# Performance work log

Measured on AMD Instinct MI355X. Metric: run time of the kernel, lower is better.

## Reference

```python
import jax, jax.numpy as jnp
import numpy as np

CONF = 0.25
IOU = 0.7
MAX_DET = 300
IMG_H = 1280
IMG_W = 1280
KPT_SHAPE = (17, 3)
MAX_NMS = 3000
BS = 16
N_ANCH = 33600  # (1280/8)^2 + (1280/16)^2 + (1280/32)^2


def setup_inputs() -> dict:
    key = jax.random.key(0)
    k1, k2, k3, k4 = jax.random.split(key, 4)
    # realistic YOLO head outputs: centers in image, positive w/h, conf in (0,1)
    cxy = jax.random.uniform(k1, (BS, 2, N_ANCH)) * jnp.array([IMG_W, IMG_H], jnp.float32).reshape(1, 2, 1)
    wh = jax.random.uniform(k2, (BS, 2, N_ANCH)) * 200.0 + 4.0
    conf = jax.random.uniform(k3, (BS, 1, N_ANCH))
    kpts = jax.random.uniform(k4, (BS, 51, N_ANCH)) * float(IMG_W)
    preds = jnp.concatenate([cxy, wh, conf, kpts], axis=1).astype(jnp.float32)
    return {"preds": preds}


def _pairwise_iou(boxes):
    # boxes: [M, 4] xyxy
    area = (boxes[:, 2] - boxes[:, 0]) * (boxes[:, 3] - boxes[:, 1])
    lt = jnp.maximum(boxes[:, None, :2], boxes[None, :, :2])
    rb = jnp.minimum(boxes[:, None, 2:], boxes[None, :, 2:])
    wh = jnp.clip(rb - lt, 0.0)
    inter = wh[..., 0] * wh[..., 1]
    return inter / (area[:, None] + area[None, :] - inter + 1e-9)


def _nms_keep(boxes, valid):
    # greedy NMS over score-descending boxes; returns bool keep mask [M]
    M = boxes.shape[0]
    idx = jnp.arange(M)
    supp = (_pairwise_iou(boxes) > IOU) & (idx[None, :] > idx[:, None])

    def body(i, keep):
        # row i suppresses later boxes only if it is itself kept
        return keep & ~(supp[i] & keep[i])

    return jax.lax.fori_loop(0, M, body, valid)


def _per_image(boxes_xywh, scores, kpts):
    # boxes_xywh: [N,4], scores: [N], kpts: [N,51]
    valid = scores > CONF
    masked = jnp.where(valid, scores, -1.0)
    order = jnp.argsort(-masked)[:MAX_NMS]  # top max_nms by score, desc
    b = boxes_xywh[order]
    sc = scores[order]
    kp = kpts[order]
    v = valid[order]
    # xywh -> xyxy with clip to image bounds
    cx, cy, w, h = b[:, 0], b[:, 1], b[:, 2], b[:, 3]
    x1 = jnp.clip(cx - w / 2, 0.0, IMG_W)
    y1 = jnp.clip(cy - h / 2, 0.0, IMG_H)
    x2 = jnp.clip(cx + w / 2, 0.0, IMG_W)
    y2 = jnp.clip(cy + h / 2, 0.0, IMG_H)
    bxy = jnp.stack([x1, y1, x2, y2], axis=-1)
    # faithful to original _clip_coords quirk: only channels 0 and 1 of the 51 clipped
    kp = kp.at[:, 0].set(jnp.clip(kp[:, 0], 0.0, IMG_W))
    kp = kp.at[:, 1].set(jnp.clip(kp[:, 1], 0.0, IMG_H))
    keep = _nms_keep(bxy, v)
    rank = jnp.cumsum(keep) - 1
    sel = keep & (rank < MAX_DET)
    tgt = jnp.where(sel, rank, MAX_DET)  # dropped rows scatter to slot MAX_DET (sliced off)
    ob = jnp.zeros((MAX_DET + 1, 4), bxy.dtype).at[tgt].set(jnp.where(sel[:, None], bxy, 0.0))[:MAX_DET]
    osc = jnp.zeros((MAX_DET + 1, 1), sc.dtype).at[tgt].set(jnp.where(sel[:, None], sc[:, None], 0.0))[:MAX_DET]
    okp = jnp.zeros((MAX_DET + 1, 51), kp.dtype).at[tgt].set(jnp.where(sel[:, None], kp, 0.0))[:MAX_DET]
    return ob, osc, okp


def reference(preds):
    bs = preds.shape[0]
    x = jnp.transpose(preds, (0, 2, 1))  # [bs, N, 56]
    ob, osc, okp = jax.vmap(_per_image)(x[..., :4], x[..., 4], x[..., 5:])
    return ob, osc, okp.reshape(bs, MAX_DET, *KPT_SHAPE)
```

## Files before the change

### kernel.cpp

```cpp
#include <hip/hip_runtime.h>
#include <stdint.h>

#define N_ANCH 33600
#define BS 16
#define NCH 56
#define MAX_NMS 3000
#define MAX_DET 300
#define CONF_T 0.25f
#define IOU_T 0.7f
#define IMG 1280.0f
#define NW 47
#define NBINS 4096
#define HIST_BINS 4097
#define CAP 4096
#define WCAP 4096
#define WC_STRIDE 16
#define NIT 9

#define OFF_CAND 0
#define OFF_WL   (OFF_CAND + BS*CAP*8)
#define OFF_META (OFF_WL + BS*WCAP*4)
#define OFF_BOX  ((OFF_META + BS*MAX_NMS*8 + 15) & ~15)
#define OFF_WC   (OFF_BOX + BS*MAX_NMS*16)
#define OFF_GBM  (OFF_WC + BS*WC_STRIDE*4)
#define OFF_FOI  (OFF_GBM + BS*8)

__device__ __forceinline__ int score_bucket(float c, uint32_t* bits_out) {
    if (!(c > CONF_T)) { *bits_out = 0u; return 0; }
    uint32_t bits = __float_as_uint(c);
    *bits_out = bits;
    int bucket = (int)(bits >> 12) - 0x3E800 + 1;
    bucket = bucket < 1 ? 1 : (bucket > NBINS ? NBINS : bucket);
    return bucket;
}

__device__ __forceinline__ float iou_pair(float4 bi, float ai, float4 bj) {
    float aj  = (bj.z - bj.x) * (bj.w - bj.y);
    float ltx = fmaxf(bi.x, bj.x), lty = fmaxf(bi.y, bj.y);
    float rbx = fminf(bi.z, bj.z), rby = fminf(bi.w, bj.w);
    float wx  = fmaxf(rbx - ltx, 0.f), wy = fmaxf(rby - lty, 0.f);
    float inter = wx * wy;
    return inter / (ai + aj - inter + 1e-9f);
}

__device__ __forceinline__ unsigned long long readlane64(unsigned long long v, int lane) {
    uint32_t lo = (uint32_t)v, hi = (uint32_t)(v >> 32);
    uint32_t rlo = __builtin_amdgcn_readlane(lo, lane);
    uint32_t rhi = __builtin_amdgcn_readlane(hi, lane);
    return ((unsigned long long)rhi << 32) | (unsigned long long)rlo;
}

__global__ void __launch_bounds__(1024)
k_phase1(const float* __restrict__ preds,
         unsigned long long* __restrict__ cand,
         unsigned int* __restrict__ wlist, int* __restrict__ wcount,
         int2* __restrict__ gbm) {
    __shared__ int hl[HIST_BINS];
    __shared__ int st[HIST_BINS];
    __shared__ int part[256];
    __shared__ int suf[256];
    __shared__ int ldsB, ldsM, ldsWc;
    const int b = blockIdx.x, t = threadIdx.x;
    if (t == 0) ldsWc = 0;
    for (int i = t; i < HIST_BINS; i += 1024) hl[i] = 0;
    __syncthreads();
    const float4* conf4 = (const float4*)(preds + (size_t)b * NCH * N_ANCH + 4 * N_ANCH);
    float4 rc[NIT];
    #pragma unroll
    for (int it = 0; it < NIT; it++) {
        int a4 = t + it * 1024;
        if (a4 < N_ANCH / 4) {
            float4 c4 = conf4[a4];
            rc[it] = c4;
            uint32_t bits;
            int bk;
            bk = score_bucket(c4.x, &bits); if (bk > 0) atomicAdd(&hl[bk], 1);
            bk = score_bucket(c4.y, &bits); if (bk > 0) atomicAdd(&hl[bk], 1);
            bk = score_bucket(c4.z, &bits); if (bk > 0) atomicAdd(&hl[bk], 1);
            bk = score_bucket(c4.w, &bits); if (bk > 0) atomicAdd(&hl[bk], 1);
        }
    }
    __syncthreads();
    if (t < 256) {
        int s = 0;
        for (int k = 0; k < 16; k++) s += hl[1 + t * 16 + k];
        part[t] = s;
    }
    __syncthreads();
    if (t < 64) {
        int p0 = part[4 * t + 0], p1 = part[4 * t + 1];
        int p2 = part[4 * t + 2], p3 = part[4 * t + 3];
        int loc = p0 + p1 + p2 + p3;
        int v = loc;
        #pragma unroll
        for (int off = 1; off < 64; off <<= 1) {
            int src = t + off;
            int o = __shfl(v, src & 63);
            if (src < 64) v += o;
        }
        int above = v - loc;
        suf[4 * t + 0] = above + p1 + p2 + p3;
        suf[4 * t + 1] = above + p2 + p3;
        suf[4 * t + 2] = above + p3;
        suf[4 * t + 3] = above;
        if (t == 0) {
            if (v < MAX_NMS) { ldsB = 1; ldsM = v; }
        }
    }
    __syncthreads();
    if (t < 256) {
        int run = suf[t];
        bool maycross = (run < MAX_NMS) && (run + part[t] >= MAX_NMS);
        bool done = false;
        for (int k = 15; k >= 0; k--) {
            int bin = 1 + t * 16 + k;
            st[bin] = run;
            run += hl[bin];
            if (maycross && !done && run >= MAX_NMS) { ldsB = bin; ldsM = run; done = true; }
        }
    }
    __syncthreads();
    const int B = ldsB;
    if (t < 256) {
        for (int k = 0; k < 16; k++) {
            int bin = 1 + t * 16 + k;
            int c = hl[bin], s = st[bin];
            if (c > 0 && bin >= B && s < MAX_NMS) {
                int idx = atomicAdd(&ldsWc, 1);
                wlist[b * WCAP + idx] = (unsigned int)s | ((unsigned int)c << 16);
            }
        }
    }
    __syncthreads();
    #pragma unroll
    for (int it = 0; it < NIT; it++) {
        int a4 = t + it * 1024;
        if (a4 < N_ANCH / 4) {
            float4 c4 = rc[it];
            float cv[4] = {c4.x, c4.y, c4.z, c4.w};
            #pragma unroll
            for (int q = 0; q < 4; q++) {
                uint32_t bits;
                int bucket = score_bucket(cv[q], &bits);
                if (bucket >= B && bucket > 0) {
                    int pos = atomicAdd(&st[bucket], 1);
                    if (pos < CAP) {
                        int a = a4 * 4 + q;
                        cand[b * CAP + pos] =
                            ((unsigned long long)bits << 32) | (uint32_t)(~(uint32_t)a);
                    }
                }
            }
        }
    }
    if (t == 0) {
        wcount[b * WC_STRIDE] = ldsWc;
        gbm[b] = make_int2(ldsB, ldsM);
    }
}

__global__ void k_rank(const float* __restrict__ preds,
                       const unsigned long long* __restrict__ cand,
                       const unsigned int* __restrict__ wlist,
                       const int* __restrict__ wcount,
                       uint2* __restrict__ meta, float4* __restrict__ box_ws) {
    const int b = blockIdx.x;
    const int wc = wcount[b * WC_STRIDE];
    const int wv = blockIdx.y * (blockDim.x >> 6) + (threadIdx.x >> 6);
    const int lane = threadIdx.x & 63;
    const int wstride = gridDim.y * (blockDim.x >> 6);
    const float* pr = preds + (size_t)b * NCH * N_ANCH;
    for (int e = wv; e < wc; e += wstride) {
        unsigned int ent = wlist[b * WCAP + e];
        int s = (int)(ent & 0xffffu);
        int n = (int)(ent >> 16);
        if (s + n > CAP) n = CAP - s;
        const unsigned long long* seg = cand + b * CAP + s;
        for (int i = lane; i < n; i += 64) {
            unsigned long long ke = seg[i];
            int r = 0;
            for (int j = 0; j < n; j++) r += (seg[j] > ke);
            int pos = s + r;
            if (pos < MAX_NMS) {
                int oi = (int)(~(uint32_t)ke);
                uint32_t sbits = (uint32_t)(ke >> 32);
                float cx = pr[0 * N_ANCH + oi], cy = pr[1 * N_ANCH + oi];
                float w  = pr[2 * N_ANCH + oi], h  = pr[3 * N_ANCH + oi];
                float4 bx;
                bx.x = fminf(fmaxf(cx - w * 0.5f, 0.f), IMG);
                bx.y = fminf(fmaxf(cy - h * 0.5f, 0.f), IMG);
                bx.z = fminf(fmaxf(cx + w * 0.5f, 0.f), IMG);
                bx.w = fminf(fmaxf(cy + h * 0.5f, 0.f), IMG);
                box_ws[b * MAX_NMS + pos] = bx;
                meta[b * MAX_NMS + pos] = make_uint2((unsigned int)oi, sbits);
            }
        }
    }
}

__global__ void __launch_bounds__(1024)
k_nms(const float4* __restrict__ box_ws, const uint2* __restrict__ meta,
      const int2* __restrict__ gbm, int* __restrict__ foi, float* __restrict__ out) {
    __shared__ float4 lbox[MAX_NMS];
    __shared__ float4 kbox[MAX_DET];
    __shared__ float  karea[MAX_DET];
    __shared__ int    lsel[MAX_DET];
    __shared__ unsigned long long pres[NW];
    __shared__ unsigned long long diag[64];
    __shared__ unsigned long long keptmask_sh;
    const int b = blockIdx.x, t = threadIdx.x;
    const int M = gbm[b].y;
    const int Mc = M < MAX_NMS ? M : MAX_NMS;
    for (int j = t; j < Mc; j += 1024) lbox[j] = box_ws[b * MAX_NMS + j];
    if (t < NW) {
        int base = t * 64;
        int lo = Mc - base;
        unsigned long long inv = (lo <= 0) ? ~0ull : (lo >= 64 ? 0ull : ~((1ull << lo) - 1ull));
        pres[t] = inv;
    }
    __syncthreads();
    int kc = 0;
    const int nch = (Mc + 63) >> 6;
    for (int c = 0; c < nch && kc < MAX_DET; c++) {
        int base = c * 64;
        if (t < 64) diag[t] = 0ull;
        __syncthreads();
        {
            int jl = t >> 4, kk = t & 15;
            int j = base + jl;
            if (j < Mc && kc > 0) {
                float4 bj = lbox[j];
                bool sup = false;
                for (int kidx = kk; kidx < kc; kidx += 16) {
                    if (iou_pair(kbox[kidx], karea[kidx], bj) > IOU_T) { sup = true; break; }
                }
                if (sup) atomicOr(&pres[c], 1ull << jl);
            }
        }
        {
            int il = t >> 4;
            int j0 = (t & 15) * 4;
            int i = base + il;
            if (i < Mc) {
                float4 bi = lbox[i];
                float ai = (bi.z - bi.x) * (bi.w - bi.y);
                unsigned long long m = 0ull;
                for (int q = 0; q < 4; q++) {
                    int jl = j0 + q, j = base + jl;
                    if (j > i && j < Mc) {
                        if (iou_pair(bi, ai, lbox[j]) > IOU_T) m |= 1ull << jl;
                    }
                }
                if (m) atomicOr(&diag[il], m);
            }
        }
        __syncthreads();
        if (t < 64) {
            unsigned long long mydiag = diag[t];
            unsigned long long s = pres[c];
            unsigned long long keptm = 0ull;
            int room = MAX_DET - kc;
            int jmax = Mc - base; if (jmax > 64) jmax = 64;
            for (int bb = 0; bb < jmax; bb++) {
                if (!((s >> bb) & 1ull)) {
                    s |= readlane64(mydiag, bb);
                    keptm |= 1ull << bb;
                    if (--room == 0) break;
                }
            }
            if (t == 0) keptmask_sh = keptm;
        }
        __syncthreads();
        unsigned long long keptm = keptmask_sh;
        if (t < 64 && ((keptm >> t) & 1ull)) {
            int pos = kc + __popcll(keptm & ((1ull << t) - 1ull));
            float4 bx = lbox[base + t];
            kbox[pos] = bx;
            karea[pos] = (bx.z - bx.x) * (bx.w - bx.y);
            lsel[pos] = base + t;
        }
        kc += __popcll(keptm);
        __syncthreads();
    }
    float* ob  = out;
    float* osc = out + BS * MAX_DET * 4;
    for (int r = t; r < MAX_DET; r += 1024) {
        int det = b * MAX_DET + r;
        if (r < kc) {
            float4 bx = kbox[r];
            ob[det * 4 + 0] = bx.x; ob[det * 4 + 1] = bx.y;
            ob[det * 4 + 2] = bx.z; ob[det * 4 + 3] = bx.w;
            uint2 mt = meta[b * MAX_NMS + lsel[r]];
            osc[det] = __uint_as_float(mt.y);
            foi[det] = (int)mt.x;
        } else {
            ob[det * 4 + 0] = 0.f; ob[det * 4 + 1] = 0.f;
            ob[det * 4 + 2] = 0.f; ob[det * 4 + 3] = 0.f;
            osc[det] = 0.f;
            foi[det] = -1;
        }
    }
}

__global__ void k_kpt(const float* __restrict__ preds, const int* __restrict__ foi,
                      float* __restrict__ out) {
    int g = blockIdx.x * blockDim.x + threadIdx.x;
    int det = g >> 6, lane = g & 63;
    if (det >= BS * MAX_DET || lane >= 51) return;
    int b = det / MAX_DET;
    float* okp = out + BS * MAX_DET * 5;
    int oi = foi[det];
    if (oi >= 0) {
        float v = preds[(size_t)b * NCH * N_ANCH + (size_t)(5 + lane) * N_ANCH + oi];
        if (lane < 2) v = fminf(fmaxf(v, 0.f), IMG);
        okp[det * 51 + lane] = v;
    } else {
        okp[det * 51 + lane] = 0.f;
    }
}

extern "C" void kernel_launch(void* const* d_in, const int* in_sizes, int n_in,
                              void* d_out, int out_size, void* d_ws, size_t ws_size,
                              hipStream_t stream) {
    const float* preds = (const float*)d_in[0];
    float* out = (float*)d_out;
    char* ws = (char*)d_ws;
    unsigned long long* cand = (unsigned long long*)(ws + OFF_CAND);
    unsigned int* wlist = (unsigned int*)(ws + OFF_WL);
    uint2* meta = (uint2*)(ws + OFF_META);
    float4* box = (float4*)(ws + OFF_BOX);
    int* wcount = (int*)(ws + OFF_WC);
    int2* gbm = (int2*)(ws + OFF_GBM);
    int* foi = (int*)(ws + OFF_FOI);

    k_phase1<<<BS, 1024, 0, stream>>>(preds, cand, wlist, wcount, gbm);
    k_rank<<<dim3(BS, 32), 256, 0, stream>>>(preds, cand, wlist, wcount, meta, box);
    k_nms<<<BS, 1024, 0, stream>>>(box, meta, gbm, foi, out);
    k_kpt<<<(BS * MAX_DET * 64 + 255) / 256, 256, 0, stream>>>(preds, foi, out);
}
```

Baseline: 226.6 us.

## Fuse rank and NMS kernels via last-block-done counter; compact keypoint gather

Merges the rank/box-decode kernel into the NMS kernel. Each image now gets 8 blocks of 1024 threads that do the ranking work, and the last block to finish, detected with an atomic counter and threadfence, runs the greedy NMS. This removes one kernel launch and its inter-kernel gap. The keypoint kernel now maps threads densely to the 51 channels instead of padding to 64 lanes, which removes idle lanes. The cost is a global atomic handshake, a counter reset in phase1, and the large NMS shared-memory footprint on every rank block, which may limit occupancy.

```diff
diff --git a/kernel.cpp b/kernel.cpp
--- a/kernel.cpp
+++ b/kernel.cpp
@@ -16,6 +16,7 @@
 #define WCAP 4096
 #define WC_STRIDE 16
 #define NIT 9
+#define RNB 8
 
 #define OFF_CAND 0
 #define OFF_WL   (OFF_CAND + BS*CAP*8)
@@ -24,6 +25,7 @@
 #define OFF_WC   (OFF_BOX + BS*MAX_NMS*16)
 #define OFF_GBM  (OFF_WC + BS*WC_STRIDE*4)
 #define OFF_FOI  (OFF_GBM + BS*8)
+#define OFF_DONE (OFF_FOI + BS*MAX_DET*4)
 
 __device__ __forceinline__ int score_bucket(float c, uint32_t* bits_out) {
     if (!(c > CONF_T)) { *bits_out = 0u; return 0; }
@@ -54,14 +56,14 @@
 k_phase1(const float* __restrict__ preds,
          unsigned long long* __restrict__ cand,
          unsigned int* __restrict__ wlist, int* __restrict__ wcount,
-         int2* __restrict__ gbm) {
+         int2* __restrict__ gbm, int* __restrict__ done) {
     __shared__ int hl[HIST_BINS];
     __shared__ int st[HIST_BINS];
     __shared__ int part[256];
     __shared__ int suf[256];
     __shared__ int ldsB, ldsM, ldsWc;
     const int b = blockIdx.x, t = threadIdx.x;
-    if (t == 0) ldsWc = 0;
+    if (t == 0) { ldsWc = 0; done[b] = 0; }
     for (int i = t; i < HIST_BINS; i += 1024) hl[i] = 0;
     __syncthreads();
     const float4* conf4 = (const float4*)(preds + (size_t)b * NCH * N_ANCH + 4 * N_ANCH);
@@ -111,12 +113,12 @@
     if (t < 256) {
         int run = suf[t];
         bool maycross = (run < MAX_NMS) && (run + part[t] >= MAX_NMS);
-        bool done = false;
+        bool done_ = false;
         for (int k = 15; k >= 0; k--) {
             int bin = 1 + t * 16 + k;
             st[bin] = run;
             run += hl[bin];
-            if (maycross && !done && run >= MAX_NMS) { ldsB = bin; ldsM = run; done = true; }
+            if (maycross && !done_ && run >= MAX_NMS) { ldsB = bin; ldsM = run; done_ = true; }
         }
     }
     __syncthreads();
@@ -159,48 +161,14 @@
     }
 }
 
-__global__ void k_rank(const float* __restrict__ preds,
-                       const unsigned long long* __restrict__ cand,
-                       const unsigned int* __restrict__ wlist,
-                       const int* __restrict__ wcount,
-                       uint2* __restrict__ meta, float4* __restrict__ box_ws) {
-    const int b = blockIdx.x;
-    const int wc = wcount[b * WC_STRIDE];
-    const int wv = blockIdx.y * (blockDim.x >> 6) + (threadIdx.x >> 6);
-    const int lane = threadIdx.x & 63;
-    const int wstride = gridDim.y * (blockDim.x >> 6);
-    const float* pr = preds + (size_t)b * NCH * N_ANCH;
-    for (int e = wv; e < wc; e += wstride) {
-        unsigned int ent = wlist[b * WCAP + e];
-        int s = (int)(ent & 0xffffu);
-        int n = (int)(ent >> 16);
-        if (s + n > CAP) n = CAP - s;
-        const unsigned long long* seg = cand + b * CAP + s;
-        for (int i = lane; i < n; i += 64) {
-            unsigned long long ke = seg[i];
-            int r = 0;
-            for (int j = 0; j < n; j++) r += (seg[j] > ke);
-            int pos = s + r;
-            if (pos < MAX_NMS) {
-                int oi = (int)(~(uint32_t)ke);
-                uint32_t sbits = (uint32_t)(ke >> 32);
-                float cx = pr[0 * N_ANCH + oi], cy = pr[1 * N_ANCH + oi];
-                float w  = pr[2 * N_ANCH + oi], h  = pr[3 * N_ANCH + oi];
-                float4 bx;
-                bx.x = fminf(fmaxf(cx - w * 0.5f, 0.f), IMG);
-                bx.y = fminf(fmaxf(cy - h * 0.5f, 0.f), IMG);
-                bx.z = fminf(fmaxf(cx + w * 0.5f, 0.f), IMG);
-                bx.w = fminf(fmaxf(cy + h * 0.5f, 0.f), IMG);
-                box_ws[b * MAX_NMS + pos] = bx;
-                meta[b * MAX_NMS + pos] = make_uint2((unsigned int)oi, sbits);
-            }
-        }
-    }
-}
-
 __global__ void __launch_bounds__(1024)
-k_nms(const float4* __restrict__ box_ws, const uint2* __restrict__ meta,
-      const int2* __restrict__ gbm, int* __restrict__ foi, float* __restrict__ out) {
+k_ranknms(const float* __restrict__ preds,
+          const unsigned long long* __restrict__ cand,
+          const unsigned int* __restrict__ wlist,
+          const int* __restrict__ wcount,
+          uint2* __restrict__ meta, float4* __restrict__ box_ws,
+          const int2* __restrict__ gbm, int* __restrict__ done,
+          int* __restrict__ foi, float* __restrict__ out) {
     __shared__ float4 lbox[MAX_NMS];
     __shared__ float4 kbox[MAX_DET];
     __shared__ float  karea[MAX_DET];
@@ -208,7 +176,50 @@
     __shared__ unsigned long long pres[NW];
     __shared__ unsigned long long diag[64];
     __shared__ unsigned long long keptmask_sh;
+    __shared__ int lastFlag;
     const int b = blockIdx.x, t = threadIdx.x;
+    {
+        const int wc = wcount[b * WC_STRIDE];
+        const int wv = blockIdx.y * 16 + (t >> 6);
+        const int lane = t & 63;
+        const float* pr = preds + (size_t)b * NCH * N_ANCH;
+        for (int e = wv; e < wc; e += RNB * 16) {
+            unsigned int ent = wlist[b * WCAP + e];
+            int s = (int)(ent & 0xffffu);
+            int n = (int)(ent >> 16);
+            if (s + n > CAP) n = CAP - s;
+            const unsigned long long* seg = cand + b * CAP + s;
+            for (int i = lane; i < n; i += 64) {
+                unsigned long long ke = seg[i];
+                int r = 0;
+                for (int j = 0; j < n; j++) r += (seg[j] > ke);
+                int pos = s + r;
+                if (pos < MAX_NMS) {
+                    int oi = (int)(~(uint32_t)ke);
+                    uint32_t sbits = (uint32_t)(ke >> 32);
+                    float cx = pr[0 * N_ANCH + oi], cy = pr[1 * N_ANCH + oi];
+                    float w  = pr[2 * N_ANCH + oi], h  = pr[3 * N_ANCH + oi];
+                    float4 bx;
+                    bx.x = fminf(fmaxf(cx - w * 0.5f, 0.f), IMG);
+                    bx.y = fminf(fmaxf(cy - h * 0.5f, 0.f), IMG);
+                    bx.z = fminf(fmaxf(cx + w * 0.5f, 0.f), IMG);
+                    bx.w = fminf(fmaxf(cy + h * 0.5f, 0.f), IMG);
+                    box_ws[b * MAX_NMS + pos] = bx;
+                    meta[b * MAX_NMS + pos] = make_uint2((unsigned int)oi, sbits);
+                }
+            }
+        }
+    }
+    __syncthreads();
+    if (t == 0) {
+        __threadfence();
+        lastFlag = (atomicAdd(&done[b], 1) == RNB - 1);
+    }
+    __syncthreads();
+    if (!lastFlag) return;
+    if (t == 0) __threadfence();
+    __syncthreads();
+
     const int M = gbm[b].y;
     const int Mc = M < MAX_NMS ? M : MAX_NMS;
     for (int j = t; j < Mc; j += 1024) lbox[j] = box_ws[b * MAX_NMS + j];
@@ -305,18 +316,17 @@
 __global__ void k_kpt(const float* __restrict__ preds, const int* __restrict__ foi,
                       float* __restrict__ out) {
     int g = blockIdx.x * blockDim.x + threadIdx.x;
-    int det = g >> 6, lane = g & 63;
-    if (det >= BS * MAX_DET || lane >= 51) return;
+    if (g >= BS * MAX_DET * 51) return;
+    int det = g / 51, lane = g - det * 51;
     int b = det / MAX_DET;
     float* okp = out + BS * MAX_DET * 5;
     int oi = foi[det];
+    float v = 0.f;
     if (oi >= 0) {
-        float v = preds[(size_t)b * NCH * N_ANCH + (size_t)(5 + lane) * N_ANCH + oi];
+        v = preds[(size_t)b * NCH * N_ANCH + (size_t)(5 + lane) * N_ANCH + oi];
         if (lane < 2) v = fminf(fmaxf(v, 0.f), IMG);
-        okp[det * 51 + lane] = v;
-    } else {
-        okp[det * 51 + lane] = 0.f;
-    }
+    }
+    okp[g] = v;
 }
 
 extern "C" void kernel_launch(void* const* d_in, const int* in_sizes, int n_in,
@@ -332,9 +342,10 @@
     int* wcount = (int*)(ws + OFF_WC);
     int2* gbm = (int2*)(ws + OFF_GBM);
     int* foi = (int*)(ws + OFF_FOI);
-
-    k_phase1<<<BS, 1024, 0, stream>>>(preds, cand, wlist, wcount, gbm);
-    k_rank<<<dim3(BS, 32), 256, 0, stream>>>(preds, cand, wlist, wcount, meta, box);
-    k_nms<<<BS, 1024, 0, stream>>>(box, meta, gbm, foi, out);
-    k_kpt<<<(BS * MAX_DET * 64 + 255) / 256, 256, 0, stream>>>(preds, foi, out);
-}
+    int* done = (int*)(ws + OFF_DONE);
+
+    k_phase1<<<BS, 1024, 0, stream>>>(preds, cand, wlist, wcount, gbm, done);
+    k_ranknms<<<dim3(BS, RNB), 1024, 0, stream>>>(preds, cand, wlist, wcount,
+                                                  meta, box, gbm, done, foi, out);
+    k_kpt<<<(BS * MAX_DET * 51 + 255) / 256, 256, 0, stream>>>(preds, foi, out);
+}
```

After: 230.2 us. Within noise of the previous version (+1.6%).
